# Performance work log

Measured on AMD Instinct MI355X. Metric: run time of the kernel, lower is better.

The kernel has to match this reference:

```python
import jax, jax.numpy as jnp
import numpy as np

# LinearMoELayer(input_size=2048, output_size=2048, num_experts=8, num_selects=2,
#                bias=True, gate_network='mlp', gate_use_balance=True,
#                gate_add_noise=True, gate_use_softmax=True)
# Eval-mode forward semantics (deterministic: noise branch only active in training).
B, S, D, O, E, K = 4, 2048, 2048, 2048, 8, 2
BAL_W = 1e-2   # balance_loss_weight
EPS = 1e-10    # cv_squared eps


def setup_inputs() -> dict:
    key = jax.random.key(0)
    ks = jax.random.split(key, 5)
    x = jax.random.normal(ks[0], (B, S, D), dtype=jnp.float32)
    # gate 'mlp': Linear(D,E,bias=False) -> tanh -> Linear(E,E,bias=False)
    gate_w1 = jax.random.normal(ks[1], (E, D), dtype=jnp.float32) * (1.0 / np.sqrt(D))
    gate_w2 = jax.random.normal(ks[2], (E, E), dtype=jnp.float32) * (1.0 / np.sqrt(E))
    # LinearExperts: per-expert weight [E, O, D] and bias [E, O] (F.linear convention)
    expert_w = jax.random.normal(ks[3], (E, O, D), dtype=jnp.float32) * (1.0 / np.sqrt(D))
    expert_b = jax.random.normal(ks[4], (E, O), dtype=jnp.float32) * 0.01
    return {"x": x, "gate_w1": gate_w1, "gate_w2": gate_w2,
            "expert_w": expert_w, "expert_b": expert_b}


def _cv_squared(v):
    # torch: v.var() / (v.mean()**2 + eps); torch.var is unbiased (ddof=1)
    m = jnp.mean(v)
    var = jnp.sum((v - m) ** 2) / (v.shape[0] - 1)
    return var / (m * m + EPS)


def reference(x, gate_w1, gate_w2, expert_w, expert_b):
    xt = x.reshape(-1, D)                                  # [T, D]
    T = xt.shape[0]
    # --- TopKBalancedNoisyGate (eval path) ---
    logits = jnp.tanh(xt @ gate_w1.T) @ gate_w2.T          # [T, E]
    top_logits, top_idx = jax.lax.top_k(logits, K)         # [T, K]
    scores = jax.nn.softmax(top_logits.astype(jnp.float32), axis=-1)  # [T, K]
    # scatter top-k scores into dense [T, E] gate matrix
    dense = jnp.zeros((T, E), dtype=scores.dtype)
    dense = dense.at[jnp.arange(T)[:, None], top_idx].set(scores)
    importance = dense.sum(axis=0)                         # [E]
    load = (dense > 0).sum(axis=0).astype(jnp.float32)     # [E] token counts
    gate_loss = BAL_W * (_cv_squared(importance) + _cv_squared(load))
    # --- UniversalCalculator: per-expert linear + score-weighted combine ---
    # math-equivalent to sort/dispatch/grouped-linear/index_add combine
    h = jnp.einsum('td,eod->teo', xt, expert_w) + expert_b[None, :, :]  # [T, E, O]
    y = jnp.einsum('te,teo->to', dense, h)                 # [T, O]
    return y.reshape(B, S, O), gate_loss
```

## Files before the change

kernel.cpp:

```cpp
#include <hip/hip_runtime.h>
#include <hip/hip_bf16.h>

#define TT 8192
#define DD 2048
#define OO 2048
#define EE 8

typedef __attribute__((ext_vector_type(4))) float f32x4;
typedef __attribute__((ext_vector_type(8))) short s16x8;
typedef __attribute__((ext_vector_type(4))) short s16x4;

__device__ __forceinline__ short f2bf(float f) {
    union { float f; unsigned u; } v; v.f = f;
    unsigned r = (v.u + 0x7FFFu + ((v.u >> 16) & 1u)) >> 16;
    return (short)(unsigned short)r;
}
__device__ __forceinline__ float bf2f(short s) {
    union { unsigned u; float f; } v; v.u = ((unsigned)(unsigned short)s) << 16;
    return v.f;
}

__global__ __launch_bounds__(256) void cvt_both_kernel(
    const float* __restrict__ ew, short* __restrict__ wbf, long n8w,
    const float* __restrict__ x, short* __restrict__ xbf, long n8x)
{
    long i = (long)blockIdx.x * blockDim.x + threadIdx.x;
    long stride = (long)gridDim.x * blockDim.x;
    long total = n8w + n8x;
    for (; i < total; i += stride) {
        const float* in; short* out; long k;
        if (i < n8w) { in = ew; out = wbf; k = i; }
        else         { in = x;  out = xbf; k = i - n8w; }
        f32x4 a = ((const f32x4*)in)[k * 2];
        f32x4 b = ((const f32x4*)in)[k * 2 + 1];
        s16x8 r;
        r[0] = f2bf(a[0]); r[1] = f2bf(a[1]); r[2] = f2bf(a[2]); r[3] = f2bf(a[3]);
        r[4] = f2bf(b[0]); r[5] = f2bf(b[1]); r[6] = f2bf(b[2]); r[7] = f2bf(b[3]);
        ((s16x8*)out)[k] = r;
    }
}

__global__ __launch_bounds__(256) void gate_kernel(
    const float* __restrict__ x, const float* __restrict__ w1, const float* __restrict__ w2,
    int* __restrict__ tk_idx, float* __restrict__ tk_score)
{
    const int lane = threadIdx.x & 63;
    const int wid = threadIdx.x >> 6;
    const int t = blockIdx.x * 4 + wid;
    const float* xt = x + (long)t * DD;

    float acc[8] = {0.f,0.f,0.f,0.f,0.f,0.f,0.f,0.f};
#pragma unroll
    for (int i = 0; i < DD / 256; ++i) {
        f32x4 xv = *(const f32x4*)&xt[i * 256 + lane * 4];
#pragma unroll
        for (int e2 = 0; e2 < 8; ++e2) {
            f32x4 wv = *(const f32x4*)&w1[e2 * DD + i * 256 + lane * 4];
            acc[e2] += xv[0]*wv[0] + xv[1]*wv[1] + xv[2]*wv[2] + xv[3]*wv[3];
        }
    }
#pragma unroll
    for (int e2 = 0; e2 < 8; ++e2) {
#pragma unroll
        for (int off = 32; off > 0; off >>= 1)
            acc[e2] += __shfl_xor(acc[e2], off, 64);
    }

    float th[8], lg[8];
#pragma unroll
    for (int e2 = 0; e2 < 8; ++e2) th[e2] = tanhf(acc[e2]);
#pragma unroll
    for (int eo = 0; eo < 8; ++eo) {
        float s = 0.f;
#pragma unroll
        for (int e2 = 0; e2 < 8; ++e2) s += th[e2] * w2[eo * 8 + e2];
        lg[eo] = s;
    }
    int e0 = 0;
#pragma unroll
    for (int q = 1; q < 8; ++q) if (lg[q] > lg[e0]) e0 = q;
    int e1 = (e0 == 0) ? 1 : 0;
#pragma unroll
    for (int q = 0; q < 8; ++q) if (q != e0 && lg[q] > lg[e1]) e1 = q;

    float d = expf(lg[e1] - lg[e0]);
    float s0 = 1.f / (1.f + d);
    float s1 = d / (1.f + d);

    if (lane == 0) {
        tk_idx[t * 2] = e0; tk_idx[t * 2 + 1] = e1;
        tk_score[t * 2] = s0; tk_score[t * 2 + 1] = s1;
    }
}

__global__ __launch_bounds__(256) void build_lists(
    const int* __restrict__ tk_idx, const float* __restrict__ tk_score,
    int* __restrict__ tok_list, float* __restrict__ score_list, int* __restrict__ cnt,
    float* __restrict__ imp)
{
    const int e = blockIdx.x;
    const int lane = threadIdx.x & 63;
    const int wid = threadIdx.x >> 6;
    __shared__ int wsum[4];
    __shared__ float wsumF[4];
    int base = 0;
    float ssum = 0.f;
    for (int t0 = 0; t0 < TT; t0 += 256) {
        int t = t0 + threadIdx.x;
        int i0 = tk_idx[t * 2], i1 = tk_idx[t * 2 + 1];
        bool has = (i0 == e) || (i1 == e);
        int slot = (i0 == e) ? 0 : 1;
        float sc = (i0 == e) ? tk_score[t * 2] : tk_score[t * 2 + 1];
        unsigned long long m = __ballot(has);
        int prefix = __popcll(m & ((1ull << lane) - 1ull));
        if (lane == 0) wsum[wid] = __popcll(m);
        __syncthreads();
        int woff = 0;
#pragma unroll
        for (int w = 0; w < 4; ++w) woff += (w < wid) ? wsum[w] : 0;
        int total = wsum[0] + wsum[1] + wsum[2] + wsum[3];
        if (has) {
            int p = base + woff + prefix;
            tok_list[e * TT + p] = t * 2 + slot;
            score_list[e * TT + p] = sc;
            ssum += sc;
        }
        base += total;
        __syncthreads();
    }
#pragma unroll
    for (int off = 32; off > 0; off >>= 1)
        ssum += __shfl_xor(ssum, off, 64);
    if (lane == 0) wsumF[wid] = ssum;
    __syncthreads();
    if (threadIdx.x == 0) {
        cnt[e] = base;
        imp[e] = wsumF[0] + wsumF[1] + wsumF[2] + wsumF[3];
    }
}

__global__ __launch_bounds__(256) void combine_kernel(float* __restrict__ y,
                                                      const short* __restrict__ part0,
                                                      const short* __restrict__ part1,
                                                      const float* __restrict__ imp,
                                                      const int* __restrict__ cnt) {
    if (blockIdx.x == 0 && threadIdx.x == 0) {
        float im[8], ld[8];
        float mi = 0.f, ml = 0.f;
#pragma unroll
        for (int q = 0; q < 8; ++q) {
            im[q] = imp[q]; ld[q] = (float)cnt[q];
            mi += im[q]; ml += ld[q];
        }
        mi *= 0.125f; ml *= 0.125f;
        float vi = 0.f, vl = 0.f;
#pragma unroll
        for (int q = 0; q < 8; ++q) {
            float a = im[q] - mi; vi += a * a;
            float b = ld[q] - ml; vl += b * b;
        }
        vi /= 7.f; vl /= 7.f;
        y[(size_t)TT * OO] = 0.01f * (vi / (mi * mi + 1e-10f) + vl / (ml * ml + 1e-10f));
    }
    long i = (long)blockIdx.x * blockDim.x + threadIdx.x;
    long stride = (long)gridDim.x * blockDim.x;
    const long n4 = (long)TT * OO / 4;
    for (; i < n4; i += stride) {
        s16x4 p0 = ((const s16x4*)part0)[i];
        s16x4 p1 = ((const s16x4*)part1)[i];
        f32x4 v;
        v[0] = bf2f(p0[0]) + bf2f(p1[0]);
        v[1] = bf2f(p0[1]) + bf2f(p1[1]);
        v[2] = bf2f(p0[2]) + bf2f(p1[2]);
        v[3] = bf2f(p0[3]) + bf2f(p1[3]);
        ((f32x4*)y)[i] = v;
    }
}

#define GLD16(gsrc, ldst) \
    __builtin_amdgcn_global_load_lds((const __attribute__((address_space(1))) unsigned int*)(gsrc), \
                                     (__attribute__((address_space(3))) unsigned int*)(ldst), 16, 0, 0)

#define BAR() __builtin_amdgcn_s_barrier()

__global__ __launch_bounds__(512, 2) void moe_gemm(
    const short* __restrict__ xbf, const short* __restrict__ wbf,
    const float* __restrict__ eb,
    const int* __restrict__ tok_list, const float* __restrict__ score_list,
    const int* __restrict__ cnt, short* __restrict__ part0, short* __restrict__ part1)
{
    const int e = blockIdx.z;
    const int n_e = cnt[e];
    const int xb = blockIdx.x, yb = blockIdx.y;
    const int cb = ((xb >> 2) << 2) + (yb & 3);
    const int rb = (xb & 3) + ((yb >> 2) << 2);
    const int row0 = rb * 256;
    if (row0 >= n_e) return;
    const int col0 = cb * 256;

    __shared__ alignas(16) short lds[2 * 32768];
    __shared__ int   stok[256];
    __shared__ float ssc[256];

    const int tid = threadIdx.x;
    const int lane = tid & 63;
    const int wid = tid >> 6;
    const int wr = wid >> 2, wc = wid & 3;
    const int fr = lane & 15, fq = lane >> 4;
    const char* ldsb = (const char*)lds;

    if (tid < 256) {
        int slot = row0 + tid;
        if (slot >= n_e) slot = n_e - 1;
        stok[tid] = tok_list[e * TT + slot];
        ssc[tid]  = score_list[e * TT + slot];
    }
    __syncthreads();

    const int r_ = tid >> 3;
    const int csw = ((tid & 7) ^ (r_ & 7)) * 8;
    const short* aS[4];
#pragma unroll
    for (int g = 0; g < 4; ++g)
        aS[g] = xbf + (long)(stok[g * 64 + r_] >> 1) * DD + csw;
    const short* bS[4];
#pragma unroll
    for (int g = 0; g < 4; ++g)
        bS[g] = wbf + (long)e * OO * DD + (long)(col0 + g * 64 + r_) * DD + csw;

#define STAGE_A(g, kt) GLD16(aS[g] + (kt) * 64, (char*)lds + ((kt) & 1) * 65536 + ((g) * 512 + tid) * 16)
#define STAGE_B(g, kt) GLD16(bS[g] + (kt) * 64, (char*)lds + ((kt) & 1) * 65536 + 32768 + ((g) * 512 + tid) * 16)

    const int aBase = (wr * 128 + fr) * 128;
    const int bBase = 32768 + (wc * 64 + fr) * 128;
    const int sw0 = (fq ^ (fr & 7)) * 16;
    const int sw1 = ((fq + 4) ^ (fr & 7)) * 16;

    f32x4 acc[8][4];
#pragma unroll
    for (int m = 0; m < 8; ++m)
#pragma unroll
        for (int n = 0; n < 4; ++n) acc[m][n] = f32x4{0.f, 0.f, 0.f, 0.f};

    STAGE_A(0, 0); STAGE_A(1, 0); STAGE_A(2, 0); STAGE_A(3, 0);
    STAGE_B(0, 0); STAGE_B(1, 0); STAGE_B(2, 0); STAGE_B(3, 0);
    asm volatile("s_waitcnt vmcnt(0)");
    BAR();

#pragma unroll 1
    for (int j = 0; j < DD / 64; ++j) {
        const int fb = (j & 1) * 65536;
        const bool st1 = (j + 1) < DD / 64;

        s16x8 a0[4][2], a1[4][2], bb[4][2];

#pragma unroll
        for (int mm = 0; mm < 4; ++mm) {
            a0[mm][0] = *(const s16x8*)(ldsb + fb + aBase + mm * 2048 + sw0);
            a0[mm][1] = *(const s16x8*)(ldsb + fb + aBase + mm * 2048 + sw1);
        }
#pragma unroll
        for (int n = 0; n < 4; ++n) {
            bb[n][0] = *(const s16x8*)(ldsb + fb + bBase + n * 2048 + sw0);
            bb[n][1] = *(const s16x8*)(ldsb + fb + bBase + n * 2048 + sw1);
        }
        if (st1) {
            STAGE_A(0, j + 1); STAGE_A(1, j + 1);
            STAGE_A(2, j + 1); STAGE_A(3, j + 1);
            STAGE_B(0, j + 1); STAGE_B(1, j + 1);
            STAGE_B(2, j + 1); STAGE_B(3, j + 1);
        }
        __builtin_amdgcn_s_setprio(1);
#pragma unroll
        for (int mm = 0; mm < 4; ++mm)
#pragma unroll
            for (int n = 0; n < 4; ++n) {
                acc[mm][n] = __builtin_amdgcn_mfma_f32_16x16x32_bf16(a0[mm][0], bb[n][0], acc[mm][n], 0, 0, 0);
                acc[mm][n] = __builtin_amdgcn_mfma_f32_16x16x32_bf16(a0[mm][1], bb[n][1], acc[mm][n], 0, 0, 0);
            }
        __builtin_amdgcn_s_setprio(0);
#pragma unroll
        for (int mm = 0; mm < 4; ++mm) {
            a1[mm][0] = *(const s16x8*)(ldsb + fb + aBase + 8192 + mm * 2048 + sw0);
            a1[mm][1] = *(const s16x8*)(ldsb + fb + aBase + 8192 + mm * 2048 + sw1);
        }
        __builtin_amdgcn_s_setprio(1);
#pragma unroll
        for (int mm = 0; mm < 4; ++mm)
#pragma unroll
            for (int n = 0; n < 4; ++n) {
                acc[4 + mm][n] = __builtin_amdgcn_mfma_f32_16x16x32_bf16(a1[mm][0], bb[n][0], acc[4 + mm][n], 0, 0, 0);
                acc[4 + mm][n] = __builtin_amdgcn_mfma_f32_16x16x32_bf16(a1[mm][1], bb[n][1], acc[4 + mm][n], 0, 0, 0);
            }
        __builtin_amdgcn_s_setprio(0);

        asm volatile("s_waitcnt lgkmcnt(0)");
        __builtin_amdgcn_sched_barrier(0);
        asm volatile("s_waitcnt vmcnt(0)");
        __builtin_amdgcn_sched_barrier(0);
        BAR();
    }

    float bval[4];
#pragma unroll
    for (int n = 0; n < 4; ++n)
        bval[n] = eb[e * OO + col0 + wc * 64 + n * 16 + fr];

#pragma unroll
    for (int m = 0; m < 8; ++m) {
#pragma unroll
        for (int jj = 0; jj < 4; ++jj) {
            int tslot = wr * 128 + m * 16 + fq * 4 + jj;
            if (row0 + tslot < n_e) {
                int packed = stok[tslot];
                int t = packed >> 1;
                float s = ssc[tslot];
                short* dst = ((packed & 1) == 0) ? part0 : part1;
#pragma unroll
                for (int n = 0; n < 4; ++n) {
                    int o = col0 + wc * 64 + n * 16 + fr;
                    dst[(long)t * OO + o] = f2bf(s * (acc[m][n][jj] + bval[n]));
                }
            }
        }
    }
#undef STAGE_A
#undef STAGE_B
}

extern "C" void kernel_launch(void* const* d_in, const int* in_sizes, int n_in,
                              void* d_out, int out_size, void* d_ws, size_t ws_size,
                              hipStream_t stream) {
    const float* x  = (const float*)d_in[0];
    const float* w1 = (const float*)d_in[1];
    const float* w2 = (const float*)d_in[2];
    const float* ew = (const float*)d_in[3];
    const float* eb = (const float*)d_in[4];
    float* y = (float*)d_out;

    char* ws = (char*)d_ws;
    short* xbf = (short*)ws;            ws += (size_t)TT * DD * 2;
    short* wbf = (short*)ws;            ws += (size_t)EE * OO * DD * 2;
    short* part0 = (short*)ws;          ws += (size_t)TT * OO * 2;
    short* part1 = (short*)ws;          ws += (size_t)TT * OO * 2;
    int*   tok_list = (int*)ws;         ws += (size_t)EE * TT * 4;
    float* score_list = (float*)ws;     ws += (size_t)EE * TT * 4;
    int*   tk_idx = (int*)ws;           ws += (size_t)TT * 2 * 4;
    float* tk_score = (float*)ws;       ws += (size_t)TT * 2 * 4;
    int*   cnt = (int*)ws;              ws += 64;
    float* imp = (float*)ws;            ws += 64;

    cvt_both_kernel<<<8192, 256, 0, stream>>>(ew, wbf, (long)EE * OO * DD / 8,
                                              x, xbf, (long)TT * DD / 8);
    gate_kernel<<<TT / 4, 256, 0, stream>>>(x, w1, w2, tk_idx, tk_score);
    build_lists<<<EE, 256, 0, stream>>>(tk_idx, tk_score, tok_list, score_list, cnt, imp);
    moe_gemm<<<dim3(8, 32, EE), 512, 0, stream>>>(
        xbf, wbf, eb, tok_list, score_list, cnt, part0, part1);
    combine_kernel<<<2048, 256, 0, stream>>>(y, part0, part1, imp, cnt);
}
```

Measured before the change: 286.4 us.

## Triple-buffer gathered A tiles to prefetch two K-steps ahead

The A (gathered token rows) tiles move to a 3-slot LDS ring and are prefetched two iterations ahead, while B stays double-buffered one step ahead. The wait now leaves the latest A loads in flight instead of draining vmcnt to zero each iteration. This aims to hide the latency of the irregular gather loads. It also drops the stok/ssc shared arrays and reads token ids and scores straight from global memory, in exchange for more LDS use (160KB) and repeated global index reads in the epilogue.

New measurement: 300.5 us. 1.05x slower.

```diff
diff --git a/kernel.cpp b/kernel.cpp
--- a/kernel.cpp
+++ b/kernel.cpp
@@ -198,9 +198,7 @@
     if (row0 >= n_e) return;
     const int col0 = cb * 256;
 
-    __shared__ alignas(16) short lds[2 * 32768];
-    __shared__ int   stok[256];
-    __shared__ float ssc[256];
+    __shared__ alignas(16) short lds[81920];
 
     const int tid = threadIdx.x;
     const int lane = tid & 63;
@@ -209,30 +207,25 @@
     const int fr = lane & 15, fq = lane >> 4;
     const char* ldsb = (const char*)lds;
 
-    if (tid < 256) {
-        int slot = row0 + tid;
-        if (slot >= n_e) slot = n_e - 1;
-        stok[tid] = tok_list[e * TT + slot];
-        ssc[tid]  = score_list[e * TT + slot];
-    }
-    __syncthreads();
-
     const int r_ = tid >> 3;
     const int csw = ((tid & 7) ^ (r_ & 7)) * 8;
     const short* aS[4];
 #pragma unroll
-    for (int g = 0; g < 4; ++g)
-        aS[g] = xbf + (long)(stok[g * 64 + r_] >> 1) * DD + csw;
+    for (int g = 0; g < 4; ++g) {
+        int sl = row0 + g * 64 + r_;
+        if (sl >= n_e) sl = n_e - 1;
+        aS[g] = xbf + (long)(tok_list[e * TT + sl] >> 1) * DD + csw;
+    }
     const short* bS[4];
 #pragma unroll
     for (int g = 0; g < 4; ++g)
         bS[g] = wbf + (long)e * OO * DD + (long)(col0 + g * 64 + r_) * DD + csw;
 
-#define STAGE_A(g, kt) GLD16(aS[g] + (kt) * 64, (char*)lds + ((kt) & 1) * 65536 + ((g) * 512 + tid) * 16)
-#define STAGE_B(g, kt) GLD16(bS[g] + (kt) * 64, (char*)lds + ((kt) & 1) * 65536 + 32768 + ((g) * 512 + tid) * 16)
+#define STAGE_A(g, kt) GLD16(aS[g] + (kt) * 64, (char*)lds + ((kt) % 3) * 32768 + ((g) * 512 + tid) * 16)
+#define STAGE_B(g, kt) GLD16(bS[g] + (kt) * 64, (char*)lds + 98304 + ((kt) & 1) * 32768 + ((g) * 512 + tid) * 16)
 
     const int aBase = (wr * 128 + fr) * 128;
-    const int bBase = 32768 + (wc * 64 + fr) * 128;
+    const int bBase = (wc * 64 + fr) * 128;
     const int sw0 = (fq ^ (fr & 7)) * 16;
     const int sw1 = ((fq + 4) ^ (fr & 7)) * 16;
 
@@ -244,31 +237,41 @@
 
     STAGE_A(0, 0); STAGE_A(1, 0); STAGE_A(2, 0); STAGE_A(3, 0);
     STAGE_B(0, 0); STAGE_B(1, 0); STAGE_B(2, 0); STAGE_B(3, 0);
-    asm volatile("s_waitcnt vmcnt(0)");
+    STAGE_A(0, 1); STAGE_A(1, 1); STAGE_A(2, 1); STAGE_A(3, 1);
+    asm volatile("s_waitcnt vmcnt(4)");
     BAR();
 
+    int fA = 0;
 #pragma unroll 1
     for (int j = 0; j < DD / 64; ++j) {
-        const int fb = (j & 1) * 65536;
+        const int fbA = fA * 32768;
+        const int fbB = 98304 + (j & 1) * 32768;
+        int fA2 = fA + 2; if (fA2 >= 3) fA2 -= 3;
+        const int fbA2 = fA2 * 32768;
         const bool st1 = (j + 1) < DD / 64;
+        const bool st2 = (j + 2) < DD / 64;
 
         s16x8 a0[4][2], a1[4][2], bb[4][2];
 
 #pragma unroll
         for (int mm = 0; mm < 4; ++mm) {
-            a0[mm][0] = *(const s16x8*)(ldsb + fb + aBase + mm * 2048 + sw0);
-            a0[mm][1] = *(const s16x8*)(ldsb + fb + aBase + mm * 2048 + sw1);
+            a0[mm][0] = *(const s16x8*)(ldsb + fbA + aBase + mm * 2048 + sw0);
+            a0[mm][1] = *(const s16x8*)(ldsb + fbA + aBase + mm * 2048 + sw1);
         }
 #pragma unroll
         for (int n = 0; n < 4; ++n) {
-            bb[n][0] = *(const s16x8*)(ldsb + fb + bBase + n * 2048 + sw0);
-            bb[n][1] = *(const s16x8*)(ldsb + fb + bBase + n * 2048 + sw1);
+            bb[n][0] = *(const s16x8*)(ldsb + fbB + bBase + n * 2048 + sw0);
+            bb[n][1] = *(const s16x8*)(ldsb + fbB + bBase + n * 2048 + sw1);
         }
         if (st1) {
-            STAGE_A(0, j + 1); STAGE_A(1, j + 1);
-            STAGE_A(2, j + 1); STAGE_A(3, j + 1);
             STAGE_B(0, j + 1); STAGE_B(1, j + 1);
             STAGE_B(2, j + 1); STAGE_B(3, j + 1);
+        }
+        if (st2) {
+            GLD16(aS[0] + (j + 2) * 64, (char*)lds + fbA2 + (0 * 512 + tid) * 16);
+            GLD16(aS[1] + (j + 2) * 64, (char*)lds + fbA2 + (1 * 512 + tid) * 16);
+            GLD16(aS[2] + (j + 2) * 64, (char*)lds + fbA2 + (2 * 512 + tid) * 16);
+            GLD16(aS[3] + (j + 2) * 64, (char*)lds + fbA2 + (3 * 512 + tid) * 16);
         }
         __builtin_amdgcn_s_setprio(1);
 #pragma unroll
@@ -281,8 +284,8 @@
         __builtin_amdgcn_s_setprio(0);
 #pragma unroll
         for (int mm = 0; mm < 4; ++mm) {
-            a1[mm][0] = *(const s16x8*)(ldsb + fb + aBase + 8192 + mm * 2048 + sw0);
-            a1[mm][1] = *(const s16x8*)(ldsb + fb + aBase + 8192 + mm * 2048 + sw1);
+            a1[mm][0] = *(const s16x8*)(ldsb + fbA + aBase + 8192 + mm * 2048 + sw0);
+            a1[mm][1] = *(const s16x8*)(ldsb + fbA + aBase + 8192 + mm * 2048 + sw1);
         }
         __builtin_amdgcn_s_setprio(1);
 #pragma unroll
@@ -296,9 +299,11 @@
 
         asm volatile("s_waitcnt lgkmcnt(0)");
         __builtin_amdgcn_sched_barrier(0);
-        asm volatile("s_waitcnt vmcnt(0)");
+        if (st2) { asm volatile("s_waitcnt vmcnt(4)"); }
+        else     { asm volatile("s_waitcnt vmcnt(0)"); }
         __builtin_amdgcn_sched_barrier(0);
         BAR();
+        fA = (fA == 2) ? 0 : fA + 1;
     }
 
     float bval[4];
@@ -312,9 +317,9 @@
         for (int jj = 0; jj < 4; ++jj) {
             int tslot = wr * 128 + m * 16 + fq * 4 + jj;
             if (row0 + tslot < n_e) {
-                int packed = stok[tslot];
+                int packed = tok_list[e * TT + row0 + tslot];
+                float s = score_list[e * TT + row0 + tslot];
                 int t = packed >> 1;
-                float s = ssc[tslot];
                 short* dst = ((packed & 1) == 0) ? part0 : part1;
 #pragma unroll
                 for (int n = 0; n < 4; ++n) {
```
